# Optimization experiments

Hardware: AMD Instinct MI355X
Metric: run time of the kernel (lower is better)

The kernel has to match this reference:

```python
import jax, jax.numpy as jnp
import numpy as np

B, N = 4, 1024
DIM, DEPTH, HEADS, DIM_HEAD, TCD = 512, 4, 8, 64, 512
HID = HEADS * DIM_HEAD  # 512
INNER = 4 * DIM         # 2048
MAX_REL = 32
N_REL = 2 * MAX_REL + 1  # 65
SCALE = DIM_HEAD ** -0.5
EPS = 1e-5


def setup_inputs() -> dict:
    key = jax.random.key(0)
    ks = jax.random.split(key, 16)
    s = 0.02
    inp = {
        "x": jax.random.normal(ks[0], (B, N, DIM), jnp.float32),
        "time": jax.random.normal(ks[1], (B, 1, TCD), jnp.float32),
        "seq_mask": jnp.ones((B, N), jnp.float32),
        "residue_index": jnp.tile(jnp.arange(N, dtype=jnp.int32)[None], (B, 1)),
        # relative positional encoding linear (65 -> heads)
        "relpos_w": jax.random.normal(ks[2], (N_REL, HEADS), jnp.float32) * s,
        "relpos_b": jnp.zeros((HEADS,), jnp.float32),
        # per-layer attention params (stacked over depth)
        "attn_norm_g": jnp.ones((DEPTH, DIM), jnp.float32),
        "attn_time_w": jax.random.normal(ks[3], (DEPTH, TCD, 2 * DIM), jnp.float32) * s,
        "attn_time_b": jnp.zeros((DEPTH, 2 * DIM), jnp.float32),
        "to_q_w": jax.random.normal(ks[4], (DEPTH, DIM, HID), jnp.float32) * s,
        "to_kv_w": jax.random.normal(ks[5], (DEPTH, DIM, 2 * HID), jnp.float32) * s,
        "to_out_w": jax.random.normal(ks[6], (DEPTH, HID, DIM), jnp.float32) * s,
        # per-layer feedforward params
        "ff_norm_g": jnp.ones((DEPTH, DIM), jnp.float32),
        "ff_time_w": jax.random.normal(ks[7], (DEPTH, TCD, 2 * INNER), jnp.float32) * s,
        "ff_time_b": jnp.zeros((DEPTH, 2 * INNER), jnp.float32),
        "ff_in_w": jax.random.normal(ks[8], (DEPTH, DIM, INNER), jnp.float32) * s,
        "ff_in_b": jnp.zeros((DEPTH, INNER), jnp.float32),
        "ff_out_w": jax.random.normal(ks[9], (DEPTH, INNER, DIM), jnp.float32) * s,
        "ff_out_b": jnp.zeros((DEPTH, DIM), jnp.float32),
    }
    return inp


def _ln(x, g):
    m = jnp.mean(x, axis=-1, keepdims=True)
    v = jnp.mean(jnp.square(x - m), axis=-1, keepdims=True)
    return (x - m) * jax.lax.rsqrt(v + EPS) * g


def _forward(x, time, seq_mask, residue_index, relpos_w, relpos_b,
             attn_norm_g, attn_time_w, attn_time_b, to_q_w, to_kv_w, to_out_w,
             ff_norm_g, ff_time_w, ff_time_b, ff_in_w, ff_in_b, ff_out_w, ff_out_b):
    # relative positional bias: [b, heads, i, j]
    d_ij = residue_index[:, :, None] - residue_index[:, None, :]
    idx = jnp.clip(d_ij, -MAX_REL, MAX_REL) + MAX_REL  # argmin over integer bins == clip
    bias = relpos_w[idx] + relpos_b                    # [b, i, j, h]
    bias = jnp.transpose(bias, (0, 3, 1, 2))           # [b, h, i, j]

    mask3 = seq_mask[..., None]                                       # [b, n, 1]
    pair_mask = seq_mask[:, None, :, None] * seq_mask[:, None, None, :]  # [b, 1, i, j]
    t_act = jax.nn.silu(time)                                         # [b, 1, tcd]

    x = x * mask3
    for d in range(DEPTH):
        # ---- attention block ----
        sc_sh = t_act @ attn_time_w[d] + attn_time_b[d]               # [b, 1, 2*dim]
        sc, sh = jnp.split(sc_sh, 2, axis=-1)
        xn = _ln(x, attn_norm_g[d]) * (sc + 1.0) + sh
        xn = xn * mask3
        q = (xn @ to_q_w[d]).reshape(B, N, HEADS, DIM_HEAD) * SCALE
        # NOTE: context = pre-norm x (faithful to original code)
        kv = (x @ to_kv_w[d]).reshape(B, N, 2, HEADS, DIM_HEAD)
        k, v = kv[:, :, 0], kv[:, :, 1]
        sim = jnp.einsum('bihd,bjhd->bhij', q, k) + bias
        sim = sim - (1.0 - pair_mask) * 1e6
        attn = jax.nn.softmax(sim, axis=-1)
        out = jnp.einsum('bhij,bjhd->bihd', attn, v).reshape(B, N, HID)
        out = (out @ to_out_w[d]) * mask3
        x = x + out
        # ---- feedforward block ----
        sc_sh = t_act @ ff_time_w[d] + ff_time_b[d]                   # [b, 1, 2*inner]
        sc, sh = jnp.split(sc_sh, 2, axis=-1)
        h = jax.nn.silu(_ln(x, ff_norm_g[d]) @ ff_in_w[d] + ff_in_b[d])
        h = h * (sc + 1.0) + sh
        x = x + (h @ ff_out_w[d] + ff_out_b[d])
        x = x * mask3
    return x


def reference(x, time, seq_mask, residue_index, relpos_w, relpos_b,
              attn_norm_g, attn_time_w, attn_time_b, to_q_w, to_kv_w, to_out_w,
              ff_norm_g, ff_time_w, ff_time_b, ff_in_w, ff_in_b, ff_out_w, ff_out_b):
    return _forward(x, time, seq_mask, residue_index, relpos_w, relpos_b,
                    attn_norm_g, attn_time_w, attn_time_b, to_q_w, to_kv_w, to_out_w,
                    ff_norm_g, ff_time_w, ff_time_b, ff_in_w, ff_in_b, ff_out_w, ff_out_b)
```

## Files before the change

kernel.cpp:

```cpp
#include <hip/hip_runtime.h>
#include <hip/hip_bf16.h>

constexpr int kB = 4, kN = 1024, kD = 512, kH = 8, kDh = 64, kT = 512;
constexpr int kHid = 512, kI = 2048, kRel = 65, kDepth = 4;
constexpr int kBN = kB * kN;

typedef short s16x8 __attribute__((ext_vector_type(8)));
typedef float f32x4 __attribute__((ext_vector_type(4)));

__device__ __forceinline__ float ldin(const void* p, long i, int isb) {
  if (isb) return __bfloat162float(((const __hip_bfloat16*)p)[i]);
  return ((const float*)p)[i];
}

__device__ __forceinline__ unsigned short bfbits(float v) {
  __hip_bfloat16 h = __float2bfloat16(v);
  return *(unsigned short*)&h;
}

__device__ __forceinline__ void gload16(const void* g, void* l) {
  __builtin_amdgcn_global_load_lds(
      (const __attribute__((address_space(1))) unsigned int*)g,
      (__attribute__((address_space(3))) unsigned int*)l, 16, 0, 0);
}

__global__ void k_detect(const void* __restrict__ x, int* __restrict__ flag) {
  const unsigned int* u = (const unsigned int*)x;
  unsigned int v = u[threadIdx.x];
  int e = (v >> 7) & 0xFF;
  int good = (e >= 100 && e <= 140) ? 1 : 0;
  unsigned long long m = __ballot(good);
  if (threadIdx.x == 0) flag[0] = (__popcll(m) >= 48) ? 1 : 0;
}

__global__ void k_xinit(const void* __restrict__ xin, const void* __restrict__ seqm,
                        float* __restrict__ x, __hip_bfloat16* __restrict__ xb,
                        const int* __restrict__ flag) {
  const int isb = *flag;
  const long base = ((long)blockIdx.x * 256 + threadIdx.x) * 8;
  const int row = (int)(base >> 9);
  const float mk = ldin(seqm, row, isb);
  __align__(16) unsigned short pk[8];
  #pragma unroll
  for (int j = 0; j < 8; j++) {
    float v = ldin(xin, base + j, isb) * mk;
    x[base + j] = v;
    pk[j] = bfbits(v);
  }
  *(uint4*)(xb + base) = *(const uint4*)pk;
}

__global__ __launch_bounds__(256) void k_timeproj_part(
    const void* __restrict__ timein,
    const void* __restrict__ atw, const void* __restrict__ ftw,
    float* __restrict__ part, const int* __restrict__ flag) {
  const int isb = *flag;
  __shared__ float T[kB * 64];
  const int d = blockIdx.z, kc = blockIdx.y;
  const int tt0 = kc * 64;
  {
    const int b = threadIdx.x >> 6, ttl = threadIdx.x & 63;
    const float tv = ldin(timein, (long)b * kT + tt0 + ttl, isb);
    T[b * 64 + ttl] = tv / (1.f + __expf(-tv));
  }
  __syncthreads();
  const int c = blockIdx.x * 256 + threadIdx.x;
  float a0 = 0, a1 = 0, a2 = 0, a3 = 0;
  if (c < 2 * kD) {
    const long wo = (long)d * kT * 2 * kD + (long)tt0 * 2 * kD + c;
    #pragma unroll 4
    for (int tt = 0; tt < 64; tt++) {
      const float w = ldin(atw, wo + (long)tt * 2 * kD, isb);
      a0 += T[0 * 64 + tt] * w; a1 += T[1 * 64 + tt] * w;
      a2 += T[2 * 64 + tt] * w; a3 += T[3 * 64 + tt] * w;
    }
  } else {
    const int c2 = c - 2 * kD;
    const long wo = (long)d * kT * 2 * kI + (long)tt0 * 2 * kI + c2;
    #pragma unroll 4
    for (int tt = 0; tt < 64; tt++) {
      const float w = ldin(ftw, wo + (long)tt * 2 * kI, isb);
      a0 += T[0 * 64 + tt] * w; a1 += T[1 * 64 + tt] * w;
      a2 += T[2 * 64 + tt] * w; a3 += T[3 * 64 + tt] * w;
    }
  }
  float* pp = part + ((long)(d * 8 + kc) * 4) * 5120 + c;
  pp[0] = a0; pp[5120] = a1; pp[2 * 5120] = a2; pp[3 * 5120] = a3;
}

__global__ __launch_bounds__(256) void k_timeproj_comb(
    const float* __restrict__ part,
    const void* __restrict__ atb, const void* __restrict__ ftb,
    float* __restrict__ ascsh, float* __restrict__ fscsh,
    const int* __restrict__ flag) {
  const int isb = *flag;
  const int d = blockIdx.y;
  const int c = blockIdx.x * 256 + threadIdx.x;
  float s[4] = {0, 0, 0, 0};
  #pragma unroll
  for (int kc = 0; kc < 8; kc++) {
    const float* pp = part + ((long)(d * 8 + kc) * 4) * 5120 + c;
    s[0] += pp[0]; s[1] += pp[5120]; s[2] += pp[2 * 5120]; s[3] += pp[3 * 5120];
  }
  if (c < 2 * kD) {
    const float bv = ldin(atb, (long)d * 2 * kD + c, isb);
    #pragma unroll
    for (int b = 0; b < 4; b++) ascsh[((long)d * kB + b) * 2 * kD + c] = s[b] + bv;
  } else {
    const int c2 = c - 2 * kD;
    const float bv = ldin(ftb, (long)d * 2 * kI + c2, isb);
    #pragma unroll
    for (int b = 0; b < 4; b++) fscsh[((long)d * kB + b) * 2 * kI + c2] = s[b] + bv;
  }
}

__global__ __launch_bounds__(256) void k_wtall(
    const void* __restrict__ wq, const void* __restrict__ wkv,
    const void* __restrict__ wo, const void* __restrict__ wfi,
    const void* __restrict__ wfo,
    __hip_bfloat16* __restrict__ wtq, __hip_bfloat16* __restrict__ wtkv,
    __hip_bfloat16* __restrict__ wto, __hip_bfloat16* __restrict__ wtfi,
    __hip_bfloat16* __restrict__ wtfo, const int* __restrict__ flag) {
  const int isb = *flag;
  __shared__ float T[64][65];
  const int bx = blockIdx.x;
  const void* W; __hip_bfloat16* Wt; int K, N, tl;
  if (bx < 256)       { W = wq;  Wt = wtq;  K = 512;  N = 512;  tl = bx; }
  else if (bx < 768)  { W = wkv; Wt = wtkv; K = 512;  N = 1024; tl = bx - 256; }
  else if (bx < 1024) { W = wo;  Wt = wto;  K = 512;  N = 512;  tl = bx - 768; }
  else if (bx < 2048) { W = wfi; Wt = wtfi; K = 512;  N = 2048; tl = bx - 1024; }
  else                { W = wfo; Wt = wtfo; K = 2048; N = 512;  tl = bx - 2048; }
  const int nx = N >> 6, nk = K >> 6;
  const int z = tl / (nx * nk);
  const int rem = tl % (nx * nk);
  const int k0 = (rem / nx) * 64, n0 = (rem % nx) * 64;
  const long ibase = (long)z * K * N;
  const long obase = (long)z * N * K;
  const int t = threadIdx.x;
  const int cn = t & 63, r4 = t >> 6;
  for (int rr = r4; rr < 64; rr += 4)
    T[rr][cn] = ldin(W, ibase + (long)(k0 + rr) * N + n0 + cn, isb);
  __syncthreads();
  for (int nn = r4; nn < 64; nn += 4)
    Wt[obase + (long)(n0 + nn) * K + k0 + cn] = __float2bfloat16(T[cn][nn]);
}

__global__ __launch_bounds__(256) void k_ln(
    const float* __restrict__ x, const void* __restrict__ g,
    const float* __restrict__ scsh, const void* __restrict__ seqm,
    __hip_bfloat16* __restrict__ xnb, int d, int domod, const int* __restrict__ flag) {
  const int isb = *flag;
  const int wid = threadIdx.x >> 6, lane = threadIdx.x & 63;
  const int row = blockIdx.x * 4 + wid;
  const int b = row >> 10;
  const float* xr = x + (long)row * kD + lane * 8;
  const float4 v0 = *(const float4*)xr;
  const float4 v1 = *(const float4*)(xr + 4);
  float v[8] = {v0.x, v0.y, v0.z, v0.w, v1.x, v1.y, v1.z, v1.w};
  float s = 0.f, s2 = 0.f;
  #pragma unroll
  for (int i = 0; i < 8; i++) { s += v[i]; s2 += v[i] * v[i]; }
  #pragma unroll
  for (int off = 1; off < 64; off <<= 1) { s += __shfl_xor(s, off); s2 += __shfl_xor(s2, off); }
  const float mean = s * (1.f / kD);
  const float var = fmaxf(s2 * (1.f / kD) - mean * mean, 0.f);
  const float rstd = rsqrtf(var + 1e-5f);
  float mk = 1.f;
  if (domod) mk = ldin(seqm, row, isb);
  __align__(16) unsigned short pk[8];
  #pragma unroll
  for (int i = 0; i < 8; i++) {
    const int cc = lane * 8 + i;
    float y = (v[i] - mean) * rstd * ldin(g, (long)d * kD + cc, isb);
    if (domod)
      y = (y * (scsh[(long)b * 2 * kD + cc] + 1.f) + scsh[(long)b * 2 * kD + kD + cc]) * mk;
    pk[i] = bfbits(y);
  }
  *(uint4*)(xnb + (long)row * kD + lane * 8) = *(const uint4*)pk;
}


template <int EPI>
__global__ __launch_bounds__(256) void k_mgemm(
    const __hip_bfloat16* __restrict__ A, const __hip_bfloat16* __restrict__ Wt,
    long woff, int K, int Nc,
    __hip_bfloat16* __restrict__ Cb,
    float* __restrict__ X, __hip_bfloat16* __restrict__ Xb,
    const void* __restrict__ bias, long boff,
    const float* __restrict__ scsh, const void* __restrict__ seqm,
    const int* __restrict__ flag) {
  const int isb = *flag;
  __shared__ __align__(16) short As[64 * 64];
  __shared__ __align__(16) short Bs[128 * 64];
  const int t = threadIdx.x;
  const int l = t & 63, wid = t >> 6;
  const int wm = wid & 1, wn = wid >> 1;
  const int lr = l >> 4, lc = l & 15;
  const int m0 = blockIdx.y * 64, n0 = blockIdx.x * 128;

  f32x4 acc[2][4] = {};
  const int lrow8 = l >> 3;
  const int lchunk = (l & 7) ^ lrow8;
  const __hip_bfloat16* gA = A + (long)(m0 + wid * 8 + lrow8) * K + lchunk * 8;
  const __hip_bfloat16* gB = Wt + woff + (long)(n0 + wid * 8 + lrow8) * K + lchunk * 8;

  for (int k0 = 0; k0 < K; k0 += 64) {
    #pragma unroll
    for (int p = 0; p < 2; p++)
      gload16(gA + (long)p * 32 * K + k0, As + p * 2048 + wid * 512);
    #pragma unroll
    for (int p = 0; p < 4; p++)
      gload16(gB + (long)p * 32 * K + k0, Bs + p * 2048 + wid * 512);
    __syncthreads();
    #pragma unroll
    for (int kk = 0; kk < 2; kk++) {
      s16x8 af[2], bf[4];
      #pragma unroll
      for (int fm = 0; fm < 2; fm++) {
        const int r = wm * 32 + fm * 16 + lc;
        af[fm] = *(const s16x8*)&As[r * 64 + (((kk * 4 + lr) ^ (r & 7)) * 8)];
      }
      #pragma unroll
      for (int fn = 0; fn < 4; fn++) {
        const int r = wn * 64 + fn * 16 + lc;
        bf[fn] = *(const s16x8*)&Bs[r * 64 + (((kk * 4 + lr) ^ (r & 7)) * 8)];
      }
      #pragma unroll
      for (int fm = 0; fm < 2; fm++)
        #pragma unroll
        for (int fn = 0; fn < 4; fn++)
          acc[fm][fn] = __builtin_amdgcn_mfma_f32_16x16x32_bf16(af[fm], bf[fn], acc[fm][fn], 0, 0, 0);
    }
    __syncthreads();
  }

  #pragma unroll
  for (int fm = 0; fm < 2; fm++) {
    #pragma unroll
    for (int j = 0; j < 4; j++) {
      const int r = m0 + wm * 32 + fm * 16 + lr * 4 + j;
      const int bb = r >> 10;
      float mk = 1.f;
      if constexpr (EPI == 2 || EPI == 4) mk = ldin(seqm, r, isb);
      #pragma unroll
      for (int fn = 0; fn < 4; fn++) {
        const int cc = n0 + wn * 64 + fn * 16 + lc;
        const long off = (long)r * Nc + cc;
        float v = acc[fm][fn][j];
        if constexpr (EPI == 2) {
          X[off] += v * mk;
        } else if constexpr (EPI == 3) {
          v += ldin(bias, boff + cc, isb);
          v = v / (1.f + __expf(-v));
          v = v * (scsh[(long)bb * 2 * kI + cc] + 1.f) + scsh[(long)bb * 2 * kI + kI + cc];
          Cb[off] = __float2bfloat16(v);
        } else {
          v += ldin(bias, boff + cc, isb);
          const float nx = (X[off] + v) * mk;
          X[off] = nx;
          Xb[off] = __float2bfloat16(nx);
        }
      }
    }
  }
}

__global__ __launch_bounds__(256) void k_qkv(
    const __hip_bfloat16* __restrict__ xnb, const __hip_bfloat16* __restrict__ xb,
    const __hip_bfloat16* __restrict__ wtq, const __hip_bfloat16* __restrict__ wtkv,
    __hip_bfloat16* __restrict__ qbuf, __hip_bfloat16* __restrict__ kvb) {
  constexpr int K = kD;
  __shared__ __align__(16) short As[64 * 64];
  __shared__ __align__(16) short Bs[128 * 64];
  const int t = threadIdx.x;
  const int l = t & 63, wid = t >> 6;
  const int wm = wid & 1, wn = wid >> 1;
  const int lr = l >> 4, lc = l & 15;
  const int m0 = blockIdx.y * 64;

  const __hip_bfloat16* A; const __hip_bfloat16* Wt; __hip_bfloat16* C;
  int Nc, n0; float scale;
  if (blockIdx.x < 4) {
    A = xnb; Wt = wtq; C = qbuf; Nc = kHid; n0 = blockIdx.x * 128; scale = 0.125f;
  } else {
    A = xb; Wt = wtkv; C = kvb; Nc = 2 * kHid; n0 = (blockIdx.x - 4) * 128; scale = 1.f;
  }

  f32x4 acc[2][4] = {};
  const int lrow8 = l >> 3;
  const int lchunk = (l & 7) ^ lrow8;
  const __hip_bfloat16* gA = A + (long)(m0 + wid * 8 + lrow8) * K + lchunk * 8;
  const __hip_bfloat16* gB = Wt + (long)(n0 + wid * 8 + lrow8) * K + lchunk * 8;

  for (int k0 = 0; k0 < K; k0 += 64) {
    #pragma unroll
    for (int p = 0; p < 2; p++)
      gload16(gA + (long)p * 32 * K + k0, As + p * 2048 + wid * 512);
    #pragma unroll
    for (int p = 0; p < 4; p++)
      gload16(gB + (long)p * 32 * K + k0, Bs + p * 2048 + wid * 512);
    __syncthreads();
    #pragma unroll
    for (int kk = 0; kk < 2; kk++) {
      s16x8 af[2], bf[4];
      #pragma unroll
      for (int fm = 0; fm < 2; fm++) {
        const int r = wm * 32 + fm * 16 + lc;
        af[fm] = *(const s16x8*)&As[r * 64 + (((kk * 4 + lr) ^ (r & 7)) * 8)];
      }
      #pragma unroll
      for (int fn = 0; fn < 4; fn++) {
        const int r = wn * 64 + fn * 16 + lc;
        bf[fn] = *(const s16x8*)&Bs[r * 64 + (((kk * 4 + lr) ^ (r & 7)) * 8)];
      }
      #pragma unroll
      for (int fm = 0; fm < 2; fm++)
        #pragma unroll
        for (int fn = 0; fn < 4; fn++)
          acc[fm][fn] = __builtin_amdgcn_mfma_f32_16x16x32_bf16(af[fm], bf[fn], acc[fm][fn], 0, 0, 0);
    }
    __syncthreads();
  }

  #pragma unroll
  for (int fm = 0; fm < 2; fm++)
    #pragma unroll
    for (int j = 0; j < 4; j++) {
      const int r = m0 + wm * 32 + fm * 16 + lr * 4 + j;
      #pragma unroll
      for (int fn = 0; fn < 4; fn++) {
        const int cc = n0 + wn * 64 + fn * 16 + lc;
        C[(long)r * Nc + cc] = __float2bfloat16(acc[fm][fn][j] * scale);
      }
    }
}

__global__ __launch_bounds__(256) void k_attn(
    const __hip_bfloat16* __restrict__ qb, const __hip_bfloat16* __restrict__ kvb,
    __hip_bfloat16* __restrict__ aob,
    const void* __restrict__ rpw, const void* __restrict__ rpb,
    const void* __restrict__ seqm, const int* __restrict__ ridx,
    const int* __restrict__ flag) {
  const int isb = *flag;
  const int t = threadIdx.x;
  const int i0 = blockIdx.x * 64;
  const int h = blockIdx.y;
  const int b = blockIdx.z;

  __shared__ __align__(16) short Ks[64 * 64];
  __shared__ __align__(16) short Vt[64 * 72];
  __shared__ __align__(16) short Ps[4][16 * 72];
  __shared__ float biasw[kRel];
  __shared__ int riq[64], rik[64];
  __shared__ float mkq[64], mkk[64];

  const int l = t & 63, wid = t >> 6;
  const int g = l >> 4, li = l & 15;

  if (t < kRel) biasw[t] = ldin(rpw, (long)t * kH + h, isb) + ldin(rpb, h, isb);
  if (t < 64) { riq[t] = ridx[b * kN + i0 + t]; mkq[t] = ldin(seqm, b * kN + i0 + t, isb); }

  const __hip_bfloat16* qptr =
      qb + ((long)(b * kN + i0 + wid * 16 + li)) * kHid + h * kDh + g * 8;
  s16x8 aq[2];
  aq[0] = *(const s16x8*)qptr;
  aq[1] = *(const s16x8*)(qptr + 32);

  __syncthreads();

  float mkqv[4]; int riqv[4];
  #pragma unroll
  for (int r = 0; r < 4; r++) {
    riqv[r] = riq[wid * 16 + g * 4 + r];
    mkqv[r] = mkq[wid * 16 + g * 4 + r];
  }

  float m_run[4] = {-1e30f, -1e30f, -1e30f, -1e30f};
  float l_run[4] = {0.f, 0.f, 0.f, 0.f};
  f32x4 o[4] = {};

  for (int j0 = 0; j0 < kN; j0 += 64) {
    if (t < 64) { rik[t] = ridx[b * kN + j0 + t]; mkk[t] = ldin(seqm, b * kN + j0 + t, isb); }
    #pragma unroll
    for (int p = 0; p < 2; p++) {
      const int j = p * 32 + wid * 8 + (l >> 3);
      const short* gk = (const short*)kvb + ((long)(b * kN + j0 + j)) * 1024 + h * 64 +
                        (((l & 7) ^ (l >> 3)) * 8);
      gload16(gk, Ks + p * 2048 + wid * 512);
    }
    {
      const int jv = l;
      const int d0 = wid * 16;
      const short* gv = (const short*)kvb + ((long)(b * kN + j0 + jv)) * 1024 + 512 + h * 64 + d0;
      s16x8 v0 = *(const s16x8*)gv;
      s16x8 v1 = *(const s16x8*)(gv + 8);
      #pragma unroll
      for (int dd = 0; dd < 8; dd++) {
        Vt[(d0 + dd) * 72 + jv] = v0[dd];
        Vt[(d0 + 8 + dd) * 72 + jv] = v1[dd];
      }
    }
    __syncthreads();

    f32x4 s[4] = {};
    __builtin_amdgcn_s_setprio(1);
    #pragma unroll
    for (int kc = 0; kc < 2; kc++) {
      #pragma unroll
      for (int fc = 0; fc < 4; fc++) {
        const int jl = fc * 16 + li;
        const s16x8 bk = *(const s16x8*)&Ks[jl * 64 + ((kc * 32 + g * 8) ^ ((li & 7) * 8))];
        s[fc] = __builtin_amdgcn_mfma_f32_16x16x32_bf16(aq[kc], bk, s[fc], 0, 0, 0);
      }
    }
    __builtin_amdgcn_s_setprio(0);

    int rikv[4]; float mkkv[4];
    #pragma unroll
    for (int fc = 0; fc < 4; fc++) { rikv[fc] = rik[fc * 16 + li]; mkkv[fc] = mkk[fc * 16 + li]; }
    #pragma unroll
    for (int fc = 0; fc < 4; fc++) {
      #pragma unroll
      for (int r = 0; r < 4; r++) {
        int di = riqv[r] - rikv[fc];
        di = di < -32 ? -32 : (di > 32 ? 32 : di);
        s[fc][r] += biasw[di + 32] - (1.f - mkqv[r] * mkkv[fc]) * 1e6f;
      }
    }

    #pragma unroll
    for (int r = 0; r < 4; r++) {
      float mx = fmaxf(fmaxf(s[0][r], s[1][r]), fmaxf(s[2][r], s[3][r]));
      mx = fmaxf(mx, __shfl_xor(mx, 1));
      mx = fmaxf(mx, __shfl_xor(mx, 2));
      mx = fmaxf(mx, __shfl_xor(mx, 4));
      mx = fmaxf(mx, __shfl_xor(mx, 8));
      const float m_new = fmaxf(m_run[r], mx);
      const float e = __expf(m_run[r] - m_new);
      float ps = 0.f;
      #pragma unroll
      for (int fc = 0; fc < 4; fc++) {
        const float p = __expf(s[fc][r] - m_new);
        ps += p;
        Ps[wid][(g * 4 + r) * 72 + fc * 16 + li] = (short)bfbits(p);
      }
      ps += __shfl_xor(ps, 1);
      ps += __shfl_xor(ps, 2);
      ps += __shfl_xor(ps, 4);
      ps += __shfl_xor(ps, 8);
      l_run[r] = l_run[r] * e + ps;
      m_run[r] = m_new;
      o[0][r] *= e; o[1][r] *= e; o[2][r] *= e; o[3][r] *= e;
    }

    __builtin_amdgcn_s_setprio(1);
    #pragma unroll
    for (int kc = 0; kc < 2; kc++) {
      const s16x8 pa = *(const s16x8*)&Ps[wid][li * 72 + kc * 32 + g * 8];
      #pragma unroll
      for (int fd = 0; fd < 4; fd++) {
        const s16x8 bv = *(const s16x8*)&Vt[(fd * 16 + li) * 72 + kc * 32 + g * 8];
        o[fd] = __builtin_amdgcn_mfma_f32_16x16x32_bf16(pa, bv, o[fd], 0, 0, 0);
      }
    }
    __builtin_amdgcn_s_setprio(0);
    __syncthreads();
  }

  float inv[4];
  #pragma unroll
  for (int r = 0; r < 4; r++) inv[r] = 1.f / l_run[r];
  #pragma unroll
  for (int fd = 0; fd < 4; fd++) {
    #pragma unroll
    for (int r = 0; r < 4; r++) {
      const long off =
          ((long)(b * kN + i0 + wid * 16 + g * 4 + r)) * kHid + h * kDh + fd * 16 + li;
      aob[off] = __float2bfloat16(o[fd][r] * inv[r]);
    }
  }
}

__global__ void k_out(const float* __restrict__ x, void* __restrict__ out,
                      const int* __restrict__ flag) {
  const int i = blockIdx.x * 256 + threadIdx.x;
  if (*flag) ((__hip_bfloat16*)out)[i] = __float2bfloat16(x[i]);
  else ((float*)out)[i] = x[i];
}

extern "C" void kernel_launch(void* const* d_in, const int* in_sizes, int n_in,
                              void* d_out, int out_size, void* d_ws, size_t ws_size,
                              hipStream_t stream) {
  const void* xin  = d_in[0];
  const void* timein = d_in[1];
  const void* seqm = d_in[2];
  const int*  ridx = (const int*)d_in[3];
  const void* rpw  = d_in[4];
  const void* rpb  = d_in[5];
  const void* ang  = d_in[6];
  const void* atw  = d_in[7];
  const void* atb  = d_in[8];
  const void* wq   = d_in[9];
  const void* wkv  = d_in[10];
  const void* wo   = d_in[11];
  const void* fng  = d_in[12];
  const void* ftw  = d_in[13];
  const void* ftb  = d_in[14];
  const void* wfi  = d_in[15];
  const void* bfi  = d_in[16];
  const void* wfo  = d_in[17];
  const void* bfo  = d_in[18];

  float* ws = (float*)d_ws;
  float* x     = ws;
  float* ascsh = ws + 2097152;
  float* fscsh = ws + 2113536;
  float* part  = ws + 2179072;
  int*   flag  = (int*)(ws + 2834432);
  __hip_bfloat16* bfb = (__hip_bfloat16*)(ws + 2834496);
  __hip_bfloat16* xnb  = bfb;
  __hip_bfloat16* xb   = bfb + 2097152;
  __hip_bfloat16* aob  = bfb + 4194304;
  __hip_bfloat16* hb   = bfb + 6291456;
  __hip_bfloat16* qbuf = bfb + 14680064;
  __hip_bfloat16* kvb  = bfb + 16777216;
  __hip_bfloat16* wtq  = bfb + 20971520;
  __hip_bfloat16* wtkv = bfb + 22020096;
  __hip_bfloat16* wto  = bfb + 24117248;
  __hip_bfloat16* wtfi = bfb + 25165824;
  __hip_bfloat16* wtfo = bfb + 29360128;

  k_detect<<<1, 64, 0, stream>>>(xin, flag);
  k_xinit<<<kBN * kD / 2048, 256, 0, stream>>>(xin, seqm, x, xb, flag);
  k_timeproj_part<<<dim3(20, 8, kDepth), 256, 0, stream>>>(timein, atw, ftw, part, flag);
  k_timeproj_comb<<<dim3(20, kDepth), 256, 0, stream>>>(part, atb, ftb, ascsh, fscsh, flag);
  k_wtall<<<3072, 256, 0, stream>>>(wq, wkv, wo, wfi, wfo, wtq, wtkv, wto, wtfi, wtfo, flag);

  for (int d = 0; d < kDepth; ++d) {
    k_ln<<<kBN / 4, 256, 0, stream>>>(x, ang, ascsh + (long)d * kB * 2 * kD, seqm, xnb, d, 1, flag);
    k_qkv<<<dim3(12, kBN / 64), 256, 0, stream>>>(
        xnb, xb, wtq + (long)d * kD * kHid, wtkv + (long)d * kD * 2 * kHid, qbuf, kvb);
    k_attn<<<dim3(kN / 64, kH, kB), 256, 0, stream>>>(qbuf, kvb, aob, rpw, rpb, seqm, ridx, flag);
    k_mgemm<2><<<dim3(kD / 128, kBN / 64), 256, 0, stream>>>(
        aob, wto, (long)d * kHid * kD, kHid, kD, nullptr, x, nullptr,
        nullptr, 0, nullptr, seqm, flag);
    k_ln<<<kBN / 4, 256, 0, stream>>>(x, fng, nullptr, seqm, xnb, d, 0, flag);
    k_mgemm<3><<<dim3(kI / 128, kBN / 64), 256, 0, stream>>>(
        xnb, wtfi, (long)d * kD * kI, kD, kI, hb, nullptr, nullptr,
        bfi, (long)d * kI, fscsh + (long)d * kB * 2 * kI, nullptr, flag);
    k_mgemm<4><<<dim3(kD / 128, kBN / 64), 256, 0, stream>>>(
        hb, wtfo, (long)d * kI * kD, kI, kD, nullptr, x, xb,
        bfo, (long)d * kD, nullptr, seqm, flag);
  }
  k_out<<<kBN * kD / 256, 256, 0, stream>>>(x, d_out, flag);
}
```

Measured before the change: 852.4 us.

## Double-buffer LDS tiles in GEMM and attention kernels, shrink N-tile for narrow GEMMs

Adds ping-pong LDS buffers to the GEMM, QKV and attention kernels so the next K/V or weight tile is prefetched while MFMAs run on the current one. The barrier before compute in each iteration goes away. The narrow-output GEMMs (out-projection and FF-out) now use a 64-wide N tile to launch more blocks. The attention grid is flattened with a swizzled block index that groups blocks sharing the same batch and head. LDS use roughly doubles, which may reduce occupancy.

```diff
diff --git a/kernel.cpp b/kernel.cpp
--- a/kernel.cpp
+++ b/kernel.cpp
@@ -179,8 +179,7 @@
   *(uint4*)(xnb + (long)row * kD + lane * 8) = *(const uint4*)pk;
 }
 
-
-template <int EPI>
+template <int EPI, int BN>
 __global__ __launch_bounds__(256) void k_mgemm(
     const __hip_bfloat16* __restrict__ A, const __hip_bfloat16* __restrict__ Wt,
     long woff, int K, int Nc,
@@ -189,49 +188,63 @@
     const void* __restrict__ bias, long boff,
     const float* __restrict__ scsh, const void* __restrict__ seqm,
     const int* __restrict__ flag) {
+  constexpr int FN = BN / 32;
   const int isb = *flag;
-  __shared__ __align__(16) short As[64 * 64];
-  __shared__ __align__(16) short Bs[128 * 64];
+  __shared__ __align__(16) short As[2][64 * 64];
+  __shared__ __align__(16) short Bs[2][BN * 64];
   const int t = threadIdx.x;
   const int l = t & 63, wid = t >> 6;
   const int wm = wid & 1, wn = wid >> 1;
   const int lr = l >> 4, lc = l & 15;
-  const int m0 = blockIdx.y * 64, n0 = blockIdx.x * 128;
-
-  f32x4 acc[2][4] = {};
+  const int m0 = blockIdx.y * 64, n0 = blockIdx.x * BN;
+
+  f32x4 acc[2][FN] = {};
   const int lrow8 = l >> 3;
   const int lchunk = (l & 7) ^ lrow8;
   const __hip_bfloat16* gA = A + (long)(m0 + wid * 8 + lrow8) * K + lchunk * 8;
   const __hip_bfloat16* gB = Wt + woff + (long)(n0 + wid * 8 + lrow8) * K + lchunk * 8;
 
-  for (int k0 = 0; k0 < K; k0 += 64) {
-    #pragma unroll
-    for (int p = 0; p < 2; p++)
-      gload16(gA + (long)p * 32 * K + k0, As + p * 2048 + wid * 512);
-    #pragma unroll
-    for (int p = 0; p < 4; p++)
-      gload16(gB + (long)p * 32 * K + k0, Bs + p * 2048 + wid * 512);
-    __syncthreads();
+  #pragma unroll
+  for (int p = 0; p < 2; p++)
+    gload16(gA + (long)p * 32 * K, &As[0][p * 2048 + wid * 512]);
+  #pragma unroll
+  for (int p = 0; p < FN; p++)
+    gload16(gB + (long)p * 32 * K, &Bs[0][p * 2048 + wid * 512]);
+  __syncthreads();
+
+  const int nt = K >> 6;
+  int cur = 0;
+  for (int tt = 0; tt < nt; tt++) {
+    if (tt + 1 < nt) {
+      const int k0 = (tt + 1) * 64;
+      #pragma unroll
+      for (int p = 0; p < 2; p++)
+        gload16(gA + (long)p * 32 * K + k0, &As[cur ^ 1][p * 2048 + wid * 512]);
+      #pragma unroll
+      for (int p = 0; p < FN; p++)
+        gload16(gB + (long)p * 32 * K + k0, &Bs[cur ^ 1][p * 2048 + wid * 512]);
+    }
     #pragma unroll
     for (int kk = 0; kk < 2; kk++) {
-      s16x8 af[2], bf[4];
+      s16x8 af[2], bf[FN];
       #pragma unroll
       for (int fm = 0; fm < 2; fm++) {
         const int r = wm * 32 + fm * 16 + lc;
-        af[fm] = *(const s16x8*)&As[r * 64 + (((kk * 4 + lr) ^ (r & 7)) * 8)];
-      }
-      #pragma unroll
-      for (int fn = 0; fn < 4; fn++) {
-        const int r = wn * 64 + fn * 16 + lc;
-        bf[fn] = *(const s16x8*)&Bs[r * 64 + (((kk * 4 + lr) ^ (r & 7)) * 8)];
+        af[fm] = *(const s16x8*)&As[cur][r * 64 + (((kk * 4 + lr) ^ (r & 7)) * 8)];
+      }
+      #pragma unroll
+      for (int fn = 0; fn < FN; fn++) {
+        const int r = wn * (BN / 2) + fn * 16 + lc;
+        bf[fn] = *(const s16x8*)&Bs[cur][r * 64 + (((kk * 4 + lr) ^ (r & 7)) * 8)];
       }
       #pragma unroll
       for (int fm = 0; fm < 2; fm++)
         #pragma unroll
-        for (int fn = 0; fn < 4; fn++)
+        for (int fn = 0; fn < FN; fn++)
           acc[fm][fn] = __builtin_amdgcn_mfma_f32_16x16x32_bf16(af[fm], bf[fn], acc[fm][fn], 0, 0, 0);
     }
     __syncthreads();
+    cur ^= 1;
   }
 
   #pragma unroll
@@ -243,8 +256,8 @@
       float mk = 1.f;
       if constexpr (EPI == 2 || EPI == 4) mk = ldin(seqm, r, isb);
       #pragma unroll
-      for (int fn = 0; fn < 4; fn++) {
-        const int cc = n0 + wn * 64 + fn * 16 + lc;
+      for (int fn = 0; fn < FN; fn++) {
+        const int cc = n0 + wn * (BN / 2) + fn * 16 + lc;
         const long off = (long)r * Nc + cc;
         float v = acc[fm][fn][j];
         if constexpr (EPI == 2) {
@@ -270,8 +283,8 @@
     const __hip_bfloat16* __restrict__ wtq, const __hip_bfloat16* __restrict__ wtkv,
     __hip_bfloat16* __restrict__ qbuf, __hip_bfloat16* __restrict__ kvb) {
   constexpr int K = kD;
-  __shared__ __align__(16) short As[64 * 64];
-  __shared__ __align__(16) short Bs[128 * 64];
+  __shared__ __align__(16) short As[2][64 * 64];
+  __shared__ __align__(16) short Bs[2][128 * 64];
   const int t = threadIdx.x;
   const int l = t & 63, wid = t >> 6;
   const int wm = wid & 1, wn = wid >> 1;
@@ -292,26 +305,38 @@
   const __hip_bfloat16* gA = A + (long)(m0 + wid * 8 + lrow8) * K + lchunk * 8;
   const __hip_bfloat16* gB = Wt + (long)(n0 + wid * 8 + lrow8) * K + lchunk * 8;
 
-  for (int k0 = 0; k0 < K; k0 += 64) {
-    #pragma unroll
-    for (int p = 0; p < 2; p++)
-      gload16(gA + (long)p * 32 * K + k0, As + p * 2048 + wid * 512);
-    #pragma unroll
-    for (int p = 0; p < 4; p++)
-      gload16(gB + (long)p * 32 * K + k0, Bs + p * 2048 + wid * 512);
-    __syncthreads();
+  #pragma unroll
+  for (int p = 0; p < 2; p++)
+    gload16(gA + (long)p * 32 * K, &As[0][p * 2048 + wid * 512]);
+  #pragma unroll
+  for (int p = 0; p < 4; p++)
+    gload16(gB + (long)p * 32 * K, &Bs[0][p * 2048 + wid * 512]);
+  __syncthreads();
+
+  const int nt = K >> 6;
+  int cur = 0;
+  for (int tt = 0; tt < nt; tt++) {
+    if (tt + 1 < nt) {
+      const int k0 = (tt + 1) * 64;
+      #pragma unroll
+      for (int p = 0; p < 2; p++)
+        gload16(gA + (long)p * 32 * K + k0, &As[cur ^ 1][p * 2048 + wid * 512]);
+      #pragma unroll
+      for (int p = 0; p < 4; p++)
+        gload16(gB + (long)p * 32 * K + k0, &Bs[cur ^ 1][p * 2048 + wid * 512]);
+    }
     #pragma unroll
     for (int kk = 0; kk < 2; kk++) {
       s16x8 af[2], bf[4];
       #pragma unroll
       for (int fm = 0; fm < 2; fm++) {
         const int r = wm * 32 + fm * 16 + lc;
-        af[fm] = *(const s16x8*)&As[r * 64 + (((kk * 4 + lr) ^ (r & 7)) * 8)];
+        af[fm] = *(const s16x8*)&As[cur][r * 64 + (((kk * 4 + lr) ^ (r & 7)) * 8)];
       }
       #pragma unroll
       for (int fn = 0; fn < 4; fn++) {
         const int r = wn * 64 + fn * 16 + lc;
-        bf[fn] = *(const s16x8*)&Bs[r * 64 + (((kk * 4 + lr) ^ (r & 7)) * 8)];
+        bf[fn] = *(const s16x8*)&Bs[cur][r * 64 + (((kk * 4 + lr) ^ (r & 7)) * 8)];
       }
       #pragma unroll
       for (int fm = 0; fm < 2; fm++)
@@ -320,6 +345,7 @@
           acc[fm][fn] = __builtin_amdgcn_mfma_f32_16x16x32_bf16(af[fm], bf[fn], acc[fm][fn], 0, 0, 0);
     }
     __syncthreads();
+    cur ^= 1;
   }
 
   #pragma unroll
@@ -343,16 +369,19 @@
     const int* __restrict__ flag) {
   const int isb = *flag;
   const int t = threadIdx.x;
-  const int i0 = blockIdx.x * 64;
-  const int h = blockIdx.y;
-  const int b = blockIdx.z;
-
-  __shared__ __align__(16) short Ks[64 * 64];
-  __shared__ __align__(16) short Vt[64 * 72];
+  const int bid = blockIdx.x;
+  const int swz = (bid & 7) * 64 + (bid >> 3);
+  const int x = swz & 15, h = (swz >> 4) & 7, b = swz >> 7;
+  const int i0 = x * 64;
+
+  __shared__ __align__(16) short Ks[2][64 * 64];
+  __shared__ __align__(16) short Vt[2][64 * 72];
   __shared__ __align__(16) short Ps[4][16 * 72];
   __shared__ float biasw[kRel];
-  __shared__ int riq[64], rik[64];
-  __shared__ float mkq[64], mkk[64];
+  __shared__ int riq[64];
+  __shared__ float mkq[64];
+  __shared__ int rik[2][64];
+  __shared__ float mkk[2][64];
 
   const int l = t & 63, wid = t >> 6;
   const int g = l >> 4, li = l & 15;
@@ -366,6 +395,24 @@
   aq[0] = *(const s16x8*)qptr;
   aq[1] = *(const s16x8*)(qptr + 32);
 
+  {
+    #pragma unroll
+    for (int p = 0; p < 2; p++) {
+      const int j = p * 32 + wid * 8 + (l >> 3);
+      const short* gk = (const short*)kvb + ((long)(b * kN + j)) * 1024 + h * 64 +
+                        (((l & 7) ^ (l >> 3)) * 8);
+      gload16(gk, &Ks[0][p * 2048 + wid * 512]);
+    }
+    const short* gv = (const short*)kvb + ((long)(b * kN + l)) * 1024 + 512 + h * 64 + wid * 16;
+    s16x8 v0 = *(const s16x8*)gv;
+    s16x8 v1 = *(const s16x8*)(gv + 8);
+    #pragma unroll
+    for (int dd = 0; dd < 8; dd++) {
+      Vt[0][(wid * 16 + dd) * 72 + l] = v0[dd];
+      Vt[0][(wid * 16 + 8 + dd) * 72 + l] = v1[dd];
+    }
+    if (t < 64) { rik[0][t] = ridx[b * kN + t]; mkk[0][t] = ldin(seqm, b * kN + t, isb); }
+  }
   __syncthreads();
 
   float mkqv[4]; int riqv[4];
@@ -379,28 +426,27 @@
   float l_run[4] = {0.f, 0.f, 0.f, 0.f};
   f32x4 o[4] = {};
 
-  for (int j0 = 0; j0 < kN; j0 += 64) {
-    if (t < 64) { rik[t] = ridx[b * kN + j0 + t]; mkk[t] = ldin(seqm, b * kN + j0 + t, isb); }
-    #pragma unroll
-    for (int p = 0; p < 2; p++) {
-      const int j = p * 32 + wid * 8 + (l >> 3);
-      const short* gk = (const short*)kvb + ((long)(b * kN + j0 + j)) * 1024 + h * 64 +
-                        (((l & 7) ^ (l >> 3)) * 8);
-      gload16(gk, Ks + p * 2048 + wid * 512);
-    }
-    {
-      const int jv = l;
-      const int d0 = wid * 16;
-      const short* gv = (const short*)kvb + ((long)(b * kN + j0 + jv)) * 1024 + 512 + h * 64 + d0;
-      s16x8 v0 = *(const s16x8*)gv;
-      s16x8 v1 = *(const s16x8*)(gv + 8);
-      #pragma unroll
-      for (int dd = 0; dd < 8; dd++) {
-        Vt[(d0 + dd) * 72 + jv] = v0[dd];
-        Vt[(d0 + 8 + dd) * 72 + jv] = v1[dd];
-      }
-    }
-    __syncthreads();
+  constexpr int NT = kN / 64;
+  int cur = 0;
+  for (int tt = 0; tt < NT; tt++) {
+    s16x8 nv0, nv1;
+    int nri = 0; float nmk = 0.f;
+    const bool have = (tt + 1) < NT;
+    if (have) {
+      const int j0n = (tt + 1) * 64;
+      #pragma unroll
+      for (int p = 0; p < 2; p++) {
+        const int j = p * 32 + wid * 8 + (l >> 3);
+        const short* gk = (const short*)kvb + ((long)(b * kN + j0n + j)) * 1024 + h * 64 +
+                          (((l & 7) ^ (l >> 3)) * 8);
+        gload16(gk, &Ks[cur ^ 1][p * 2048 + wid * 512]);
+      }
+      const short* gv =
+          (const short*)kvb + ((long)(b * kN + j0n + l)) * 1024 + 512 + h * 64 + wid * 16;
+      nv0 = *(const s16x8*)gv;
+      nv1 = *(const s16x8*)(gv + 8);
+      if (t < 64) { nri = ridx[b * kN + j0n + t]; nmk = ldin(seqm, b * kN + j0n + t, isb); }
+    }
 
     f32x4 s[4] = {};
     __builtin_amdgcn_s_setprio(1);
@@ -409,7 +455,7 @@
       #pragma unroll
       for (int fc = 0; fc < 4; fc++) {
         const int jl = fc * 16 + li;
-        const s16x8 bk = *(const s16x8*)&Ks[jl * 64 + ((kc * 32 + g * 8) ^ ((li & 7) * 8))];
+        const s16x8 bk = *(const s16x8*)&Ks[cur][jl * 64 + ((kc * 32 + g * 8) ^ ((li & 7) * 8))];
         s[fc] = __builtin_amdgcn_mfma_f32_16x16x32_bf16(aq[kc], bk, s[fc], 0, 0, 0);
       }
     }
@@ -417,7 +463,10 @@
 
     int rikv[4]; float mkkv[4];
     #pragma unroll
-    for (int fc = 0; fc < 4; fc++) { rikv[fc] = rik[fc * 16 + li]; mkkv[fc] = mkk[fc * 16 + li]; }
+    for (int fc = 0; fc < 4; fc++) {
+      rikv[fc] = rik[cur][fc * 16 + li];
+      mkkv[fc] = mkk[cur][fc * 16 + li];
+    }
     #pragma unroll
     for (int fc = 0; fc < 4; fc++) {
       #pragma unroll
@@ -459,12 +508,22 @@
       const s16x8 pa = *(const s16x8*)&Ps[wid][li * 72 + kc * 32 + g * 8];
       #pragma unroll
       for (int fd = 0; fd < 4; fd++) {
-        const s16x8 bv = *(const s16x8*)&Vt[(fd * 16 + li) * 72 + kc * 32 + g * 8];
+        const s16x8 bv = *(const s16x8*)&Vt[cur][(fd * 16 + li) * 72 + kc * 32 + g * 8];
         o[fd] = __builtin_amdgcn_mfma_f32_16x16x32_bf16(pa, bv, o[fd], 0, 0, 0);
       }
     }
     __builtin_amdgcn_s_setprio(0);
+
+    if (have) {
+      #pragma unroll
+      for (int dd = 0; dd < 8; dd++) {
+        Vt[cur ^ 1][(wid * 16 + dd) * 72 + l] = nv0[dd];
+        Vt[cur ^ 1][(wid * 16 + 8 + dd) * 72 + l] = nv1[dd];
+      }
+      if (t < 64) { rik[cur ^ 1][t] = nri; mkk[cur ^ 1][t] = nmk; }
+    }
     __syncthreads();
+    cur ^= 1;
   }
 
   float inv[4];
@@ -540,15 +599,15 @@
     k_ln<<<kBN / 4, 256, 0, stream>>>(x, ang, ascsh + (long)d * kB * 2 * kD, seqm, xnb, d, 1, flag);
     k_qkv<<<dim3(12, kBN / 64), 256, 0, stream>>>(
         xnb, xb, wtq + (long)d * kD * kHid, wtkv + (long)d * kD * 2 * kHid, qbuf, kvb);
-    k_attn<<<dim3(kN / 64, kH, kB), 256, 0, stream>>>(qbuf, kvb, aob, rpw, rpb, seqm, ridx, flag);
-    k_mgemm<2><<<dim3(kD / 128, kBN / 64), 256, 0, stream>>>(
+    k_attn<<<512, 256, 0, stream>>>(qbuf, kvb, aob, rpw, rpb, seqm, ridx, flag);
+    k_mgemm<2, 64><<<dim3(kD / 64, kBN / 64), 256, 0, stream>>>(
         aob, wto, (long)d * kHid * kD, kHid, kD, nullptr, x, nullptr,
         nullptr, 0, nullptr, seqm, flag);
     k_ln<<<kBN / 4, 256, 0, stream>>>(x, fng, nullptr, seqm, xnb, d, 0, flag);
-    k_mgemm<3><<<dim3(kI / 128, kBN / 64), 256, 0, stream>>>(
+    k_mgemm<3, 128><<<dim3(kI / 128, kBN / 64), 256, 0, stream>>>(
         xnb, wtfi, (long)d * kD * kI, kD, kI, hb, nullptr, nullptr,
         bfi, (long)d * kI, fscsh + (long)d * kB * 2 * kI, nullptr, flag);
-    k_mgemm<4><<<dim3(kD / 128, kBN / 64), 256, 0, stream>>>(
+    k_mgemm<4, 64><<<dim3(kD / 64, kBN / 64), 256, 0, stream>>>(
         hb, wtfo, (long)d * kI * kD, kI, kD, nullptr, x, xb,
         bfo, (long)d * kD, nullptr, seqm, flag);
   }
```

Measured after the change: 792.3 us. 7.0% less time.
